# Kernel tuning notes

Hardware: AMD Instinct MI355X
Metric: run time of the kernel (lower is better)

Reference implementation:

```python
import jax, jax.numpy as jnp
import numpy as np

L = 3; D = 128; H = 8; RBF = 16; SBF = 112
N = 60000; E = 300000; A = 8000; G = 256
EPS = 1e-8


def setup_inputs() -> dict:
    key = jax.random.key(0)
    ks = jax.random.split(key, 32)
    p = lambda i, shape: jax.random.normal(ks[i], shape, jnp.float32) * 0.05
    inp = {}
    inp['x'] = jax.random.normal(ks[0], (N, D), jnp.float32)
    inp['node_rbf'] = jax.random.uniform(ks[1], (N, RBF), jnp.float32)
    inp['edge_sbf'] = jax.random.uniform(ks[2], (E, SBF), jnp.float32)
    inp['edge_index'] = jax.random.randint(ks[3], (2, E), 0, N)
    inp['pair_atom_idx'] = jax.random.randint(ks[4], (E,), 0, A)
    inp['edge_index_0'] = jax.random.randint(ks[5], (N,), 0, A)
    inp['atom_batch'] = jnp.sort(jax.random.randint(ks[6], (A,), 0, G))
    inp['batch'] = jnp.sort(jax.random.randint(ks[7], (N,), 0, G))
    inp['edgenn_w1'] = p(8, (L, D, D)); inp['edgenn_b1'] = jnp.zeros((L, D))
    inp['edgenn_w2'] = p(9, (L, D, D)); inp['edgenn_b2'] = jnp.zeros((L, D))
    inp['conv_wq'] = p(10, (L, D, D)); inp['conv_wk'] = p(11, (L, D, D))
    inp['conv_wv'] = p(12, (L, D, D)); inp['conv_we'] = p(13, (L, D, D))
    inp['conv_wsbf'] = p(14, (L, SBF, D)); inp['conv_bsbf'] = jnp.zeros((L, D))
    inp['conv_wrbf'] = p(15, (L, RBF, D))
    inp['dense_w'] = p(16, (L, D, D)); inp['dense_b'] = jnp.zeros((L, D))
    inp['bf_w'] = p(17, (L, 2, D, D)); inp['bf_b'] = jnp.zeros((L, 2, D))
    inp['af_w'] = p(18, (L, 4, D, D)); inp['af_b'] = jnp.zeros((L, 4, D))
    inp['read_wrbf'] = p(19, (L + 1, RBF, D))
    inp['read_w1'] = p(20, (L + 1, D, D)); inp['read_b1'] = jnp.zeros((L + 1, D))
    inp['read_w2'] = p(21, (L + 1, D, D)); inp['read_b2'] = jnp.zeros((L + 1, D))
    inp['read_w3'] = p(22, (L + 1, D, 1)); inp['read_b3'] = jnp.zeros((L + 1, 1))
    return inp


def _forward(x, node_rbf, edge_sbf, edge_index, pair_atom_idx, edge_index_0,
             atom_batch, batch, edgenn_w1, edgenn_b1, edgenn_w2, edgenn_b2,
             conv_wq, conv_wk, conv_wv, conv_we, conv_wsbf, conv_bsbf, conv_wrbf,
             dense_w, dense_b, bf_w, bf_b, af_w, af_b,
             read_wrbf, read_w1, read_b1, read_w2, read_b2, read_w3, read_b3):
    segsum = jax.ops.segment_sum
    silu = jax.nn.silu
    src, dst = edge_index[0], edge_index[1]
    C = D // H

    def readout(i, h):
        # AtomWise: rbf-gated node features, scatter to atoms, small MLP -> [A,1]
        g = h * (node_rbf @ read_wrbf[i])
        atoms = segsum(g, edge_index_0, num_segments=A)
        a = silu(atoms @ read_w1[i] + read_b1[i])
        a = silu(a @ read_w2[i] + read_b2[i])
        return a @ read_w3[i] + read_b3[i]

    def res_block(h, w, b):
        # DimeNet-style ResidualLayer: x + act(lin2(act(lin1(x))))
        return h + silu(silu(h @ w[0] + b[0]) @ w[1] + b[1])

    def graph_norm(h):
        # batch-aware LayerNorm (graph mode, affine=False)
        cnt = segsum(jnp.ones((N,), h.dtype), batch, num_segments=G) * D
        mean = segsum(h.sum(-1), batch, num_segments=G) / cnt
        hc = h - mean[batch][:, None]
        var = segsum((hc * hc).sum(-1), batch, num_segments=G) / cnt
        return hc * jax.lax.rsqrt(var + EPS)[batch][:, None]

    out = x
    results = readout(0, out)
    for i in range(L):
        res0 = out
        atoms_rep = segsum(out, edge_index_0, num_segments=A)  # scatter_add to atoms
        ea = atoms_rep[pair_atom_idx]                           # gather per conv-edge
        ea = silu(ea @ edgenn_w1[i] + edgenn_b1[i]) @ edgenn_w2[i] + edgenn_b2[i]
        # SBFTransformerConv: TransformerConv with sbf-modulated messages + rbf gate
        q = (out @ conv_wq[i]).reshape(N, H, C)
        k = (out @ conv_wk[i]).reshape(N, H, C)
        v = (out @ conv_wv[i]).reshape(N, H, C)
        ek = (ea @ conv_we[i]).reshape(E, H, C)
        kj = k[src] + ek
        logit = (q[dst] * kj).sum(-1) / jnp.sqrt(jnp.asarray(C, out.dtype))  # [E,H]
        m = jax.ops.segment_max(logit, dst, num_segments=N)
        ex = jnp.exp(logit - m[dst])
        alpha = ex / (segsum(ex, dst, num_segments=N)[dst] + 1e-16)
        sw = (edge_sbf @ conv_wsbf[i] + conv_bsbf[i]).reshape(E, H, C)
        msg = (v[src] + ek) * alpha[:, :, None] * sw
        h = segsum(msg, dst, num_segments=N).reshape(N, D)
        out = h * (node_rbf @ conv_wrbf[i])
        out = graph_norm(out)
        out = res_block(out, bf_w[i], bf_b[i])
        out = silu(out @ dense_w[i] + dense_b[i])
        out = out + res0
        out = res_block(out, af_w[i, :2], af_b[i, :2])
        out = res_block(out, af_w[i, 2:], af_b[i, 2:])
        results = results + readout(i + 1, out)
    graphs = segsum(results, atom_batch, num_segments=G)  # [G,1]
    return graphs.reshape(-1) / L


def reference(x, node_rbf, edge_sbf, edge_index, pair_atom_idx, edge_index_0,
              atom_batch, batch, edgenn_w1, edgenn_b1, edgenn_w2, edgenn_b2,
              conv_wq, conv_wk, conv_wv, conv_we, conv_wsbf, conv_bsbf, conv_wrbf,
              dense_w, dense_b, bf_w, bf_b, af_w, af_b,
              read_wrbf, read_w1, read_b1, read_w2, read_b2, read_w3, read_b3):
    return _forward(x, node_rbf, edge_sbf, edge_index, pair_atom_idx, edge_index_0,
                    atom_batch, batch, edgenn_w1, edgenn_b1, edgenn_w2, edgenn_b2,
                    conv_wq, conv_wk, conv_wv, conv_we, conv_wsbf, conv_bsbf, conv_wrbf,
                    dense_w, dense_b, bf_w, bf_b, af_w, af_b,
                    read_wrbf, read_w1, read_b1, read_w2, read_b2, read_w3, read_b3)
```

## Files before the change

kernel.cpp:

```cpp
#include <hip/hip_runtime.h>
#include <math.h>

#define D    128
#define NH   8
#define CPH  16
#define RBFD 16
#define SBFD 112
#define LAYERS 3

typedef __attribute__((ext_vector_type(8))) short bf16x8;
typedef __attribute__((ext_vector_type(4))) float f32x4;

__device__ __forceinline__ float siluf(float x){ return x / (1.0f + __expf(-x)); }

__device__ __forceinline__ short f2bf(float f){
  union { float f; unsigned u; } v; v.f = f;
  unsigned r = v.u + 0x7FFFu + ((v.u >> 16) & 1u);
  return (short)(r >> 16);
}

template<int DIN, int ACT, bool GATHER, bool HASB, bool HASRES>
__global__ __launch_bounds__(256, 2) void k_gemm(
    const float* __restrict__ X, const int* __restrict__ gidx,
    const float* __restrict__ W, const float* __restrict__ bias,
    const float* res, float* __restrict__ Y, int M)
{
  __shared__ short Wt[128 * 128];
  if (DIN < 128){
    for (int i = threadIdx.x; i < 128 * 128; i += 256) Wt[i] = 0;
    __syncthreads();
  }
  for (int i = threadIdx.x; i < DIN * 128; i += 256){
    int k = i >> 7, c = i & 127;
    Wt[c * 128 + k] = f2bf(W[i]);
  }
  __syncthreads();

  const int lane = threadIdx.x & 63;
  const int wave = threadIdx.x >> 6;
  const int col0 = lane & 15;
  const int kg   = lane >> 4;

  bf16x8 Bf[8][4];
  #pragma unroll
  for (int ct = 0; ct < 8; ct++)
    #pragma unroll
    for (int s = 0; s < 4; s++)
      Bf[ct][s] = *(const bf16x8*)&Wt[(ct * 16 + col0) * 128 + s * 32 + kg * 8];

  float bs[8];
  if (HASB){
    #pragma unroll
    for (int ct = 0; ct < 8; ct++) bs[ct] = bias[ct * 16 + col0];
  }

  const long tiles = ((long)M + 63) >> 6;
  for (long t = blockIdx.x; t < tiles; t += gridDim.x){
    const long rbase = t * 64 + wave * 16;
    const long arow  = rbase + col0;
    long srow = 0;
    if (arow < M) srow = GATHER ? (long)gidx[arow] : arow;
    const float* Xp = X + srow * DIN;

    bf16x8 Af[4];
    #pragma unroll
    for (int s = 0; s < 4; s++){
      const int kb = s * 32 + kg * 8;
      bf16x8 a;
      if (DIN == 128 || kb + 8 <= DIN){
        float4 lo = *(const float4*)(Xp + kb);
        float4 hi = *(const float4*)(Xp + kb + 4);
        a[0]=f2bf(lo.x); a[1]=f2bf(lo.y); a[2]=f2bf(lo.z); a[3]=f2bf(lo.w);
        a[4]=f2bf(hi.x); a[5]=f2bf(hi.y); a[6]=f2bf(hi.z); a[7]=f2bf(hi.w);
      } else {
        #pragma unroll
        for (int j = 0; j < 8; j++) a[j] = 0;
      }
      Af[s] = a;
    }

    f32x4 acc[8];
    #pragma unroll
    for (int ct = 0; ct < 8; ct++){ acc[ct][0]=0.f; acc[ct][1]=0.f; acc[ct][2]=0.f; acc[ct][3]=0.f; }
    #pragma unroll
    for (int ct = 0; ct < 8; ct++)
      #pragma unroll
      for (int s = 0; s < 4; s++)
        acc[ct] = __builtin_amdgcn_mfma_f32_16x16x32_bf16(Af[s], Bf[ct][s], acc[ct], 0, 0, 0);

    #pragma unroll
    for (int ct = 0; ct < 8; ct++){
      const int c = ct * 16 + col0;
      #pragma unroll
      for (int r = 0; r < 4; r++){
        const long orow = rbase + kg * 4 + r;
        if (orow < M){
          float v = acc[ct][r];
          if (HASB) v += bs[ct];
          if (ACT)  v = siluf(v);
          if (HASRES) v += res[orow * D + c];
          Y[orow * D + c] = v;
        }
      }
    }
  }
}

__global__ __launch_bounds__(256, 2) void k_gemm2(
    const float* __restrict__ X, const int* __restrict__ gidx,
    const float* __restrict__ W1, const float* __restrict__ b1,
    const float* __restrict__ W2, const float* __restrict__ b2,
    float* __restrict__ Y, int M)
{
  __shared__ short W1t[128 * 128];
  __shared__ short W2t[128 * 128];
  __shared__ short Ts[64 * 128];
  for (int i = threadIdx.x; i < 128 * 128; i += 256){
    int k = i >> 7, c = i & 127;
    W1t[c * 128 + k] = f2bf(W1[i]);
    W2t[c * 128 + k] = f2bf(W2[i]);
  }
  __syncthreads();

  const int lane = threadIdx.x & 63;
  const int wave = threadIdx.x >> 6;
  const int col0 = lane & 15;
  const int kg   = lane >> 4;

  bf16x8 B1f[8][4];
  #pragma unroll
  for (int ct = 0; ct < 8; ct++)
    #pragma unroll
    for (int s = 0; s < 4; s++)
      B1f[ct][s] = *(const bf16x8*)&W1t[(ct * 16 + col0) * 128 + s * 32 + kg * 8];

  float bs1[8], bs2[8];
  #pragma unroll
  for (int ct = 0; ct < 8; ct++){ bs1[ct] = b1[ct * 16 + col0]; bs2[ct] = b2[ct * 16 + col0]; }

  const long tiles = ((long)M + 63) >> 6;
  for (long t = blockIdx.x; t < tiles; t += gridDim.x){
    const long rbase = t * 64 + wave * 16;
    const long arow  = rbase + col0;
    long srow = 0;
    if (arow < M) srow = (long)gidx[arow];
    const float* Xp = X + srow * D;

    bf16x8 Af[4];
    #pragma unroll
    for (int s = 0; s < 4; s++){
      const int kb = s * 32 + kg * 8;
      float4 lo = *(const float4*)(Xp + kb);
      float4 hi = *(const float4*)(Xp + kb + 4);
      bf16x8 a;
      a[0]=f2bf(lo.x); a[1]=f2bf(lo.y); a[2]=f2bf(lo.z); a[3]=f2bf(lo.w);
      a[4]=f2bf(hi.x); a[5]=f2bf(hi.y); a[6]=f2bf(hi.z); a[7]=f2bf(hi.w);
      Af[s] = a;
    }

    f32x4 acc[8];
    #pragma unroll
    for (int ct = 0; ct < 8; ct++){ acc[ct][0]=0.f; acc[ct][1]=0.f; acc[ct][2]=0.f; acc[ct][3]=0.f; }
    #pragma unroll
    for (int ct = 0; ct < 8; ct++)
      #pragma unroll
      for (int s = 0; s < 4; s++)
        acc[ct] = __builtin_amdgcn_mfma_f32_16x16x32_bf16(Af[s], B1f[ct][s], acc[ct], 0, 0, 0);

    #pragma unroll
    for (int ct = 0; ct < 8; ct++){
      const int c = ct * 16 + col0;
      #pragma unroll
      for (int r = 0; r < 4; r++){
        const int row = wave * 16 + kg * 4 + r;
        const int gg = (c >> 3) ^ (row & 7);
        Ts[row * 128 + gg * 8 + (c & 7)] = f2bf(siluf(acc[ct][r] + bs1[ct]));
      }
    }
    __syncthreads();

    const int row2 = wave * 16 + col0;
    bf16x8 A2f[4];
    #pragma unroll
    for (int s = 0; s < 4; s++){
      const int chunk = (s * 4 + kg) ^ (row2 & 7);
      A2f[s] = *(const bf16x8*)&Ts[row2 * 128 + chunk * 8];
    }
    __syncthreads();

    #pragma unroll
    for (int ct = 0; ct < 8; ct++){ acc[ct][0]=0.f; acc[ct][1]=0.f; acc[ct][2]=0.f; acc[ct][3]=0.f; }
    #pragma unroll
    for (int ct = 0; ct < 8; ct++){
      bf16x8 B2v[4];
      #pragma unroll
      for (int s = 0; s < 4; s++)
        B2v[s] = *(const bf16x8*)&W2t[(ct * 16 + col0) * 128 + s * 32 + kg * 8];
      #pragma unroll
      for (int s = 0; s < 4; s++)
        acc[ct] = __builtin_amdgcn_mfma_f32_16x16x32_bf16(A2f[s], B2v[s], acc[ct], 0, 0, 0);
    }

    #pragma unroll
    for (int ct = 0; ct < 8; ct++){
      const int c = ct * 16 + col0;
      #pragma unroll
      for (int r = 0; r < 4; r++){
        const long orow = rbase + kg * 4 + r;
        if (orow < M) Y[orow * D + c] = acc[ct][r] + bs2[ct];
      }
    }
  }
}

__global__ void k_hist(const int* __restrict__ idx, int* __restrict__ cnt, int M)
{
  for (long i = (long)blockIdx.x * 256 + threadIdx.x; i < M; i += (long)gridDim.x * 256)
    atomicAdd(&cnt[idx[i]], 1);
}

__global__ void k_scan(const int* __restrict__ cnt, int* __restrict__ rowptr, int M)
{
  __shared__ int buf[1024];
  const int tid = threadIdx.x;
  const int PT = 16;
  int carry = 0;
  for (int base = 0; base < M; base += 1024 * PT){
    int loc[PT]; int s = 0;
    #pragma unroll
    for (int j = 0; j < PT; j++){
      int i = base + tid * PT + j;
      loc[j] = (i < M) ? cnt[i] : 0;
      s += loc[j];
    }
    buf[tid] = s; __syncthreads();
    for (int off = 1; off < 1024; off <<= 1){
      int t = (tid >= off) ? buf[tid - off] : 0;
      __syncthreads();
      buf[tid] += t;
      __syncthreads();
    }
    int run = buf[tid] - s + carry;
    carry += buf[1023];
    __syncthreads();
    #pragma unroll
    for (int j = 0; j < PT; j++){
      int i = base + tid * PT + j;
      if (i < M) rowptr[i] = run;
      run += loc[j];
    }
  }
  if (tid == 0) rowptr[M] = carry;
}

__global__ void k_fill(const int* __restrict__ idx, const int* __restrict__ rowptr,
                       int* __restrict__ cursor, int* __restrict__ ids, int M)
{
  for (long i = (long)blockIdx.x * 256 + threadIdx.x; i < M; i += (long)gridDim.x * 256){
    int sgm = idx[i];
    int pos = atomicAdd(&cursor[sgm], 1);
    ids[rowptr[sgm] + pos] = (int)i;
  }
}

__global__ __launch_bounds__(256) void k_gather_sum(
    const float* __restrict__ X, const int* __restrict__ rowptr,
    const int* __restrict__ ids, float* __restrict__ Yat, int A_)
{
  const int lane = threadIdx.x & 63;
  const int wv   = threadIdx.x >> 6;
  for (long a = (long)blockIdx.x * 4 + wv; a < A_; a += (long)gridDim.x * 4){
    int beg = rowptr[a], end = rowptr[a + 1];
    float a0 = 0.f, a1 = 0.f;
    for (int i = beg; i < end; i++){
      const float* xp = X + (long)ids[i] * D;
      a0 += xp[lane]; a1 += xp[lane + 64];
    }
    Yat[a * D + lane] = a0; Yat[a * D + lane + 64] = a1;
  }
}

__global__ __launch_bounds__(256) void k_gather_gate_sum(
    const float* __restrict__ X, const float* __restrict__ rbf,
    const float* __restrict__ Wr, const int* __restrict__ rowptr,
    const int* __restrict__ ids, float* __restrict__ Yat, int A_)
{
  __shared__ float Wrs[RBFD * D];
  for (int i = threadIdx.x; i < RBFD * D; i += 256) Wrs[i] = Wr[i];
  __syncthreads();
  const int lane = threadIdx.x & 63;
  const int wv   = threadIdx.x >> 6;
  for (long a = (long)blockIdx.x * 4 + wv; a < A_; a += (long)gridDim.x * 4){
    int beg = rowptr[a], end = rowptr[a + 1];
    float a0 = 0.f, a1 = 0.f;
    for (int i = beg; i < end; i++){
      long n = ids[i];
      const float* xp = X + n * D;
      const float* rb = rbf + n * RBFD;
      float g0 = 0.f, g1 = 0.f;
      #pragma unroll
      for (int r = 0; r < RBFD; r++){
        float rv = rb[r];
        g0 += rv * Wrs[r * D + lane];
        g1 += rv * Wrs[r * D + lane + 64];
      }
      a0 += xp[lane] * g0; a1 += xp[lane + 64] * g1;
    }
    Yat[a * D + lane] = a0; Yat[a * D + lane + 64] = a1;
  }
}

__global__ __launch_bounds__(256) void k_attn(
    float* __restrict__ q, const float* __restrict__ k, const float* __restrict__ v,
    const float* __restrict__ ek, const float* __restrict__ sw,
    const int* __restrict__ rowptr, const int* __restrict__ eids,
    const int* __restrict__ srcA, const float* __restrict__ rbf,
    const float* __restrict__ Wr, const int* __restrict__ batch,
    double* __restrict__ sums, double* __restrict__ sumsq, int Nn)
{
  __shared__ float Wrs[RBFD * D];
  for (int i = threadIdx.x; i < RBFD * D; i += 256) Wrs[i] = Wr[i];
  __syncthreads();
  const int lane = threadIdx.x & 63;
  const int wv   = threadIdx.x >> 6;
  for (long d = (long)blockIdx.x * 4 + wv; d < Nn; d += (long)gridDim.x * 4){
    const int beg = rowptr[d], end = rowptr[d + 1];
    const float q0 = q[d * D + lane], q1 = q[d * D + lane + 64];
    float m0 = -1e30f, m1 = -1e30f, l0 = 0.f, l1 = 0.f, a0 = 0.f, a1 = 0.f;
    for (int i = beg; i < end; i++){
      const long e = eids[i];
      const long s = srcA[e];
      const float* kp = k  + s * D;
      const float* vp = v  + s * D;
      const float* ep = ek + e * D;
      const float* sp = sw + e * D;
      float e0 = ep[lane], e1 = ep[lane + 64];
      float t0 = q0 * (kp[lane] + e0), t1 = q1 * (kp[lane + 64] + e1);
      #pragma unroll
      for (int off = 1; off < 16; off <<= 1){
        t0 += __shfl_xor(t0, off, 64);
        t1 += __shfl_xor(t1, off, 64);
      }
      t0 *= 0.25f; t1 *= 0.25f;
      float u0 = (vp[lane] + e0) * sp[lane];
      float u1 = (vp[lane + 64] + e1) * sp[lane + 64];
      float nm0 = fmaxf(m0, t0), nm1 = fmaxf(m1, t1);
      float sc0 = __expf(m0 - nm0), sc1 = __expf(m1 - nm1);
      float w0 = __expf(t0 - nm0), w1 = __expf(t1 - nm1);
      l0 = l0 * sc0 + w0;  a0 = a0 * sc0 + w0 * u0;  m0 = nm0;
      l1 = l1 * sc1 + w1;  a1 = a1 * sc1 + w1 * u1;  m1 = nm1;
    }
    a0 /= (l0 + 1e-16f); a1 /= (l1 + 1e-16f);
    const float* rb = rbf + d * RBFD;
    float g0 = 0.f, g1 = 0.f;
    #pragma unroll
    for (int r = 0; r < RBFD; r++){
      float rv = rb[r];
      g0 += rv * Wrs[r * D + lane];
      g1 += rv * Wrs[r * D + lane + 64];
    }
    a0 *= g0; a1 *= g1;
    q[d * D + lane] = a0; q[d * D + lane + 64] = a1;
    float ss = a0 + a1, qq = a0 * a0 + a1 * a1;
    #pragma unroll
    for (int off = 1; off < 64; off <<= 1){
      ss += __shfl_xor(ss, off, 64);
      qq += __shfl_xor(qq, off, 64);
    }
    if (lane == 0){
      int g = batch[d];
      atomicAdd(&sums[g], (double)ss);
      atomicAdd(&sumsq[g], (double)qq);
    }
  }
}

__global__ void k_count(const int* __restrict__ batch, int* __restrict__ cnt, int M)
{
  for (long i = (long)blockIdx.x * 256 + threadIdx.x; i < M; i += (long)gridDim.x * 256)
    atomicAdd(&cnt[batch[i]], 1);
}

__global__ void k_norm_final(const double* __restrict__ sums, const double* __restrict__ sumsq,
                             const int* __restrict__ cnt, float* __restrict__ meanG,
                             float* __restrict__ rstdG)
{
  int g = threadIdx.x;
  double c = (double)cnt[g] * (double)D;
  double mean = sums[g] / c;
  double var = sumsq[g] / c - mean * mean;
  meanG[g] = (float)mean;
  rstdG[g] = (float)(1.0 / sqrt(var + 1e-8));
}

__global__ void k_norm_apply(float* __restrict__ Hio, const int* __restrict__ batch,
                             const float* __restrict__ meanG, const float* __restrict__ rstdG, int M)
{
  long total = (long)M * D;
  for (long i = (long)blockIdx.x * 256 + threadIdx.x; i < total; i += (long)gridDim.x * 256){
    long row = i >> 7;
    int g = batch[row];
    Hio[i] = (Hio[i] - meanG[g]) * rstdG[g];
  }
}

__global__ void k_dot3(const float* __restrict__ A2, const float* __restrict__ w3,
                       const float* __restrict__ b3, float* __restrict__ results, int M)
{
  int lane = threadIdx.x & 63;
  long wave = ((long)blockIdx.x * blockDim.x + threadIdx.x) >> 6;
  long nw = ((long)gridDim.x * blockDim.x) >> 6;
  for (long row = wave; row < M; row += nw){
    float a = A2[row * D + lane] * w3[lane] + A2[row * D + lane + 64] * w3[lane + 64];
    for (int off = 32; off > 0; off >>= 1) a += __shfl_down(a, off, 64);
    if (lane == 0) results[row] += a + b3[0];
  }
}

__global__ void k_final(const float* __restrict__ results, const int* __restrict__ ab,
                        float* __restrict__ out, int A_)
{
  int i = blockIdx.x * 256 + threadIdx.x;
  if (i < A_) atomicAdd(&out[ab[i]], results[i] / 3.0f);
}

__global__ void k_w2e(const float* __restrict__ w2, const float* __restrict__ we,
                      float* __restrict__ W2e)
{
  int i = blockIdx.x >> 7;
  int r = blockIdx.x & 127;
  int c = threadIdx.x;
  const float* w2p = w2 + (size_t)i * D * D + (size_t)r * D;
  const float* wep = we + (size_t)i * D * D;
  float acc = 0.f;
  for (int j = 0; j < D; j++) acc += w2p[j] * wep[j * D + c];
  W2e[(size_t)i * D * D + (size_t)r * D + c] = acc;
}

__global__ void k_b2e(const float* __restrict__ b2, const float* __restrict__ we,
                      float* __restrict__ B2e)
{
  int i = blockIdx.x; int c = threadIdx.x;
  float acc = 0.f;
  for (int j = 0; j < D; j++) acc += b2[(size_t)i * D + j] * we[(size_t)i * D * D + j * D + c];
  B2e[(size_t)i * D + c] = acc;
}

extern "C" void kernel_launch(void* const* d_in, const int* in_sizes, int n_in,
                              void* d_out, int out_size, void* d_ws, size_t ws_size,
                              hipStream_t stream)
{
  const float* x          = (const float*)d_in[0];
  const float* node_rbf   = (const float*)d_in[1];
  const float* edge_sbf   = (const float*)d_in[2];
  const int*   edge_index = (const int*)d_in[3];
  const int*   pair_idx   = (const int*)d_in[4];
  const int*   eidx0      = (const int*)d_in[5];
  const int*   atom_batch = (const int*)d_in[6];
  const int*   batch      = (const int*)d_in[7];
  const float* edgenn_w1  = (const float*)d_in[8];
  const float* edgenn_b1  = (const float*)d_in[9];
  const float* edgenn_w2  = (const float*)d_in[10];
  const float* edgenn_b2  = (const float*)d_in[11];
  const float* conv_wq    = (const float*)d_in[12];
  const float* conv_wk    = (const float*)d_in[13];
  const float* conv_wv    = (const float*)d_in[14];
  const float* conv_we    = (const float*)d_in[15];
  const float* conv_wsbf  = (const float*)d_in[16];
  const float* conv_bsbf  = (const float*)d_in[17];
  const float* conv_wrbf  = (const float*)d_in[18];
  const float* dense_w    = (const float*)d_in[19];
  const float* dense_b    = (const float*)d_in[20];
  const float* bf_w       = (const float*)d_in[21];
  const float* bf_b       = (const float*)d_in[22];
  const float* af_w       = (const float*)d_in[23];
  const float* af_b       = (const float*)d_in[24];
  const float* read_wrbf  = (const float*)d_in[25];
  const float* read_w1    = (const float*)d_in[26];
  const float* read_b1    = (const float*)d_in[27];
  const float* read_w2    = (const float*)d_in[28];
  const float* read_b2    = (const float*)d_in[29];
  const float* read_w3    = (const float*)d_in[30];
  const float* read_b3    = (const float*)d_in[31];

  const int N = in_sizes[0] / D;
  const int E = in_sizes[4];
  const int A = in_sizes[6];
  const int G = out_size;

  char* p = (char*)d_ws;
  auto carve = [&](size_t bytes)->char*{ char* r = p; p += (bytes + 255) & ~(size_t)255; return r; };
  float*    EbufA   = (float*)carve((size_t)E * D * 4);
  float*    EbufB   = (float*)carve((size_t)E * D * 4);
  float*    ping0   = (float*)carve((size_t)N * D * 4);
  float*    ping1   = (float*)carve((size_t)N * D * 4);
  float*    bq      = (float*)carve((size_t)N * D * 4);
  float*    bk      = (float*)carve((size_t)N * D * 4);
  float*    bv      = (float*)carve((size_t)N * D * 4);
  float*    bufAtoms= (float*)carve((size_t)A * D * 4);
  float*    a1      = (float*)carve((size_t)A * D * 4);
  float*    a2      = (float*)carve((size_t)A * D * 4);
  float*    results = (float*)carve((size_t)A * 4);
  double*   sumG    = (double*)carve((size_t)G * 8);
  double*   sumsqG  = (double*)carve((size_t)G * 8);
  int*      cntG    = (int*)carve((size_t)G * 4);
  float*    meanG   = (float*)carve((size_t)G * 4);
  float*    rstdG   = (float*)carve((size_t)G * 4);
  float*    W2e     = (float*)carve((size_t)LAYERS * D * D * 4);
  float*    B2e     = (float*)carve((size_t)LAYERS * D * 4);
  int*      rowptrD = (int*)carve((size_t)(N + 1) * 4);
  int*      eidsD   = (int*)carve((size_t)E * 4);
  int*      cntD    = (int*)carve((size_t)N * 4);
  int*      rowptrA = (int*)carve((size_t)(A + 1) * 4);
  int*      idsA    = (int*)carve((size_t)N * 4);
  int*      cntA    = (int*)carve((size_t)A * 4);

  const int* srcA = edge_index;
  const int* dstA = edge_index + E;

  auto ew_grid = [](long total){ long b = (total + 255) / 256; return (int)(b < 4096 ? b : 4096); };
  auto gemm_grid = [](int M){ long t = ((long)M + 63) / 64; return (int)(t < 1024 ? t : 1024); };
  const int gridAttn = (N + 3) / 4;
  const int gridAtom = (A + 3) / 4;

  hipMemsetAsync(cntG, 0, (size_t)G * 4, stream);
  hipMemsetAsync(results, 0, (size_t)A * 4, stream);
  hipMemsetAsync(d_out, 0, (size_t)G * 4, stream);
  k_count<<<ew_grid(N), 256, 0, stream>>>(batch, cntG, N);
  k_w2e<<<LAYERS * D, D, 0, stream>>>(edgenn_w2, conv_we, W2e);
  k_b2e<<<LAYERS, D, 0, stream>>>(edgenn_b2, conv_we, B2e);
  hipMemsetAsync(cntD, 0, (size_t)N * 4, stream);
  k_hist<<<ew_grid(E), 256, 0, stream>>>(dstA, cntD, E);
  k_scan<<<1, 1024, 0, stream>>>(cntD, rowptrD, N);
  hipMemsetAsync(cntD, 0, (size_t)N * 4, stream);
  k_fill<<<ew_grid(E), 256, 0, stream>>>(dstA, rowptrD, cntD, eidsD, E);
  hipMemsetAsync(cntA, 0, (size_t)A * 4, stream);
  k_hist<<<ew_grid(N), 256, 0, stream>>>(eidx0, cntA, N);
  k_scan<<<1, 1024, 0, stream>>>(cntA, rowptrA, A);
  hipMemsetAsync(cntA, 0, (size_t)A * 4, stream);
  k_fill<<<ew_grid(N), 256, 0, stream>>>(eidx0, rowptrA, cntA, idsA, N);

  auto readout = [&](int i, const float* hbuf){
    k_gather_gate_sum<<<gridAtom, 256, 0, stream>>>(hbuf, node_rbf, read_wrbf + (size_t)i * RBFD * D,
                                                    rowptrA, idsA, bufAtoms, A);
    k_gemm<D,1,false,true,false><<<gemm_grid(A),256,0,stream>>>(bufAtoms, nullptr, read_w1 + (size_t)i*D*D, read_b1 + (size_t)i*D, nullptr, a1, A);
    k_gemm<D,1,false,true,false><<<gemm_grid(A),256,0,stream>>>(a1, nullptr, read_w2 + (size_t)i*D*D, read_b2 + (size_t)i*D, nullptr, a2, A);
    k_dot3<<<((A * 64 + 255) / 256), 256, 0, stream>>>(a2, read_w3 + (size_t)i * D, read_b3 + i, results, A);
  };

  readout(0, x);

  const float* cur = x;
  float* pp[2] = {ping0, ping1};
  for (int i = 0; i < LAYERS; i++){
    float* nxt = pp[i & 1];
    const size_t oDD = (size_t)i * D * D;
    k_gather_sum<<<gridAtom, 256, 0, stream>>>(cur, rowptrA, idsA, bufAtoms, A);
    k_gemm2<<<gemm_grid(E),256,0,stream>>>(bufAtoms, pair_idx, edgenn_w1 + oDD, edgenn_b1 + (size_t)i*D,
                                           W2e + oDD, B2e + (size_t)i*D, EbufB, E);
    k_gemm<D,0,false,false,false><<<gemm_grid(N),256,0,stream>>>(cur, nullptr, conv_wq + oDD, nullptr, nullptr, bq, N);
    k_gemm<D,0,false,false,false><<<gemm_grid(N),256,0,stream>>>(cur, nullptr, conv_wk + oDD, nullptr, nullptr, bk, N);
    k_gemm<D,0,false,false,false><<<gemm_grid(N),256,0,stream>>>(cur, nullptr, conv_wv + oDD, nullptr, nullptr, bv, N);
    k_gemm<SBFD,0,false,true,false><<<gemm_grid(E),256,0,stream>>>(edge_sbf, nullptr, conv_wsbf + (size_t)i*SBFD*D, conv_bsbf + (size_t)i*D, nullptr, EbufA, E);
    hipMemsetAsync(sumG, 0, (size_t)G * 8, stream);
    hipMemsetAsync(sumsqG, 0, (size_t)G * 8, stream);
    k_attn<<<gridAttn, 256, 0, stream>>>(bq, bk, bv, EbufB, EbufA, rowptrD, eidsD, srcA,
                                         node_rbf, conv_wrbf + (size_t)i*RBFD*D, batch,
                                         sumG, sumsqG, N);
    k_norm_final<<<1, G, 0, stream>>>(sumG, sumsqG, cntG, meanG, rstdG);
    k_norm_apply<<<ew_grid((long)N * D), 256, 0, stream>>>(bq, batch, meanG, rstdG, N);
    k_gemm<D,1,false,true,false><<<gemm_grid(N),256,0,stream>>>(bq, nullptr, bf_w + (size_t)i*2*D*D, bf_b + (size_t)i*2*D, nullptr, bk, N);
    k_gemm<D,1,false,true,true ><<<gemm_grid(N),256,0,stream>>>(bk, nullptr, bf_w + (size_t)i*2*D*D + D*D, bf_b + (size_t)i*2*D + D, bq, bq, N);
    k_gemm<D,1,false,true,true ><<<gemm_grid(N),256,0,stream>>>(bq, nullptr, dense_w + oDD, dense_b + (size_t)i*D, cur, nxt, N);
    k_gemm<D,1,false,true,false><<<gemm_grid(N),256,0,stream>>>(nxt, nullptr, af_w + (size_t)i*4*D*D,         af_b + (size_t)i*4*D,       nullptr, bk, N);
    k_gemm<D,1,false,true,true ><<<gemm_grid(N),256,0,stream>>>(bk, nullptr, af_w + (size_t)i*4*D*D + D*D,   af_b + (size_t)i*4*D + D,   nxt, nxt, N);
    k_gemm<D,1,false,true,false><<<gemm_grid(N),256,0,stream>>>(nxt, nullptr, af_w + (size_t)i*4*D*D + 2*D*D, af_b + (size_t)i*4*D + 2*D, nullptr, bk, N);
    k_gemm<D,1,false,true,true ><<<gemm_grid(N),256,0,stream>>>(bk, nullptr, af_w + (size_t)i*4*D*D + 3*D*D, af_b + (size_t)i*4*D + 3*D, nxt, nxt, N);
    readout(i + 1, nxt);
    cur = nxt;
  }
  k_final<<<(A + 255) / 256, 256, 0, stream>>>(results, atom_batch, (float*)d_out, A);
}
```

Before: 3.462 ms.

## Fuse res-block GEMM pairs and readout MLP, permute edge outputs to CSR order

Result: faster. 3.255 ms (-6.0%).

```diff
diff --git a/kernel.cpp b/kernel.cpp
--- a/kernel.cpp
+++ b/kernel.cpp
@@ -19,11 +19,11 @@
   return (short)(r >> 16);
 }
 
-template<int DIN, int ACT, bool GATHER, bool HASB, bool HASRES>
+template<int DIN, int ACT, bool GATHER, bool HASB, bool HASRES, bool PERM>
 __global__ __launch_bounds__(256, 2) void k_gemm(
     const float* __restrict__ X, const int* __restrict__ gidx,
     const float* __restrict__ W, const float* __restrict__ bias,
-    const float* res, float* __restrict__ Y, int M)
+    const float* res, float* __restrict__ Y, const int* __restrict__ operm, int M)
 {
   __shared__ short Wt[128 * 128];
   if (DIN < 128){
@@ -89,18 +89,18 @@
         acc[ct] = __builtin_amdgcn_mfma_f32_16x16x32_bf16(Af[s], Bf[ct][s], acc[ct], 0, 0, 0);
 
     #pragma unroll
-    for (int ct = 0; ct < 8; ct++){
-      const int c = ct * 16 + col0;
-      #pragma unroll
-      for (int r = 0; r < 4; r++){
-        const long orow = rbase + kg * 4 + r;
-        if (orow < M){
-          float v = acc[ct][r];
-          if (HASB) v += bs[ct];
-          if (ACT)  v = siluf(v);
-          if (HASRES) v += res[orow * D + c];
-          Y[orow * D + c] = v;
-        }
+    for (int r = 0; r < 4; r++){
+      const long orow = rbase + kg * 4 + r;
+      if (orow >= M) continue;
+      const long wrow = PERM ? (long)operm[orow] : orow;
+      #pragma unroll
+      for (int ct = 0; ct < 8; ct++){
+        const int c = ct * 16 + col0;
+        float v = acc[ct][r];
+        if (HASB) v += bs[ct];
+        if (ACT)  v = siluf(v);
+        if (HASRES) v += res[orow * D + c];
+        Y[wrow * D + c] = v;
       }
     }
   }
@@ -110,7 +110,7 @@
     const float* __restrict__ X, const int* __restrict__ gidx,
     const float* __restrict__ W1, const float* __restrict__ b1,
     const float* __restrict__ W2, const float* __restrict__ b2,
-    float* __restrict__ Y, int M)
+    float* __restrict__ Y, const int* __restrict__ operm, int M)
 {
   __shared__ short W1t[128 * 128];
   __shared__ short W2t[128 * 128];
@@ -202,13 +202,242 @@
     }
 
     #pragma unroll
+    for (int r = 0; r < 4; r++){
+      const long orow = rbase + kg * 4 + r;
+      if (orow >= M) continue;
+      const long wrow = (long)operm[orow];
+      #pragma unroll
+      for (int ct = 0; ct < 8; ct++){
+        const int c = ct * 16 + col0;
+        Y[wrow * D + c] = acc[ct][r] + bs2[ct];
+      }
+    }
+  }
+}
+
+template<bool NORM>
+__global__ __launch_bounds__(256, 2) void k_res2(
+    const float* __restrict__ X,
+    const float* __restrict__ W1, const float* __restrict__ b1,
+    const float* __restrict__ W2, const float* __restrict__ b2,
+    const int* __restrict__ batch, const float* __restrict__ meanG,
+    const float* __restrict__ rstdG, float* __restrict__ Y, int M)
+{
+  __shared__ short W1t[128 * 128];
+  __shared__ short W2t[128 * 128];
+  __shared__ short Ts[64 * 128];
+  for (int i = threadIdx.x; i < 128 * 128; i += 256){
+    int k = i >> 7, c = i & 127;
+    W1t[c * 128 + k] = f2bf(W1[i]);
+    W2t[c * 128 + k] = f2bf(W2[i]);
+  }
+  __syncthreads();
+
+  const int lane = threadIdx.x & 63;
+  const int wave = threadIdx.x >> 6;
+  const int col0 = lane & 15;
+  const int kg   = lane >> 4;
+
+  bf16x8 B1f[8][4];
+  #pragma unroll
+  for (int ct = 0; ct < 8; ct++)
+    #pragma unroll
+    for (int s = 0; s < 4; s++)
+      B1f[ct][s] = *(const bf16x8*)&W1t[(ct * 16 + col0) * 128 + s * 32 + kg * 8];
+
+  float bs1[8], bs2[8];
+  #pragma unroll
+  for (int ct = 0; ct < 8; ct++){ bs1[ct] = b1[ct * 16 + col0]; bs2[ct] = b2[ct * 16 + col0]; }
+
+  const long tiles = ((long)M + 63) >> 6;
+  for (long t = blockIdx.x; t < tiles; t += gridDim.x){
+    const long rbase = t * 64 + wave * 16;
+    const long arow  = rbase + col0;
+    const float* Xp = X + (arow < M ? arow : 0) * D;
+    float xm = 0.f, xr = 1.f;
+    if (NORM && arow < M){ int g = batch[arow]; xm = meanG[g]; xr = rstdG[g]; }
+
+    bf16x8 Af[4];
+    #pragma unroll
+    for (int s = 0; s < 4; s++){
+      const int kb = s * 32 + kg * 8;
+      float4 lo = *(const float4*)(Xp + kb);
+      float4 hi = *(const float4*)(Xp + kb + 4);
+      bf16x8 a;
+      a[0]=f2bf((lo.x-xm)*xr); a[1]=f2bf((lo.y-xm)*xr); a[2]=f2bf((lo.z-xm)*xr); a[3]=f2bf((lo.w-xm)*xr);
+      a[4]=f2bf((hi.x-xm)*xr); a[5]=f2bf((hi.y-xm)*xr); a[6]=f2bf((hi.z-xm)*xr); a[7]=f2bf((hi.w-xm)*xr);
+      Af[s] = a;
+    }
+
+    f32x4 acc[8];
+    #pragma unroll
+    for (int ct = 0; ct < 8; ct++){ acc[ct][0]=0.f; acc[ct][1]=0.f; acc[ct][2]=0.f; acc[ct][3]=0.f; }
+    #pragma unroll
+    for (int ct = 0; ct < 8; ct++)
+      #pragma unroll
+      for (int s = 0; s < 4; s++)
+        acc[ct] = __builtin_amdgcn_mfma_f32_16x16x32_bf16(Af[s], B1f[ct][s], acc[ct], 0, 0, 0);
+
+    #pragma unroll
     for (int ct = 0; ct < 8; ct++){
       const int c = ct * 16 + col0;
       #pragma unroll
       for (int r = 0; r < 4; r++){
-        const long orow = rbase + kg * 4 + r;
-        if (orow < M) Y[orow * D + c] = acc[ct][r] + bs2[ct];
+        const int row = wave * 16 + kg * 4 + r;
+        const int gg = (c >> 3) ^ (row & 7);
+        Ts[row * 128 + gg * 8 + (c & 7)] = f2bf(siluf(acc[ct][r] + bs1[ct]));
       }
+    }
+    __syncthreads();
+
+    const int row2 = wave * 16 + col0;
+    bf16x8 A2f[4];
+    #pragma unroll
+    for (int s = 0; s < 4; s++){
+      const int chunk = (s * 4 + kg) ^ (row2 & 7);
+      A2f[s] = *(const bf16x8*)&Ts[row2 * 128 + chunk * 8];
+    }
+    __syncthreads();
+
+    #pragma unroll
+    for (int ct = 0; ct < 8; ct++){ acc[ct][0]=0.f; acc[ct][1]=0.f; acc[ct][2]=0.f; acc[ct][3]=0.f; }
+    #pragma unroll
+    for (int ct = 0; ct < 8; ct++){
+      bf16x8 B2v[4];
+      #pragma unroll
+      for (int s = 0; s < 4; s++)
+        B2v[s] = *(const bf16x8*)&W2t[(ct * 16 + col0) * 128 + s * 32 + kg * 8];
+      #pragma unroll
+      for (int s = 0; s < 4; s++)
+        acc[ct] = __builtin_amdgcn_mfma_f32_16x16x32_bf16(A2f[s], B2v[s], acc[ct], 0, 0, 0);
+    }
+
+    #pragma unroll
+    for (int r = 0; r < 4; r++){
+      const long orow = rbase + kg * 4 + r;
+      if (orow >= M) continue;
+      float rm = 0.f, rr = 1.f;
+      if (NORM){ int g = batch[orow]; rm = meanG[g]; rr = rstdG[g]; }
+      #pragma unroll
+      for (int ct = 0; ct < 8; ct++){
+        const int c = ct * 16 + col0;
+        float base = X[orow * D + c];
+        if (NORM) base = (base - rm) * rr;
+        Y[orow * D + c] = base + siluf(acc[ct][r] + bs2[ct]);
+      }
+    }
+  }
+}
+
+__global__ __launch_bounds__(256, 2) void k_read2(
+    const float* __restrict__ X,
+    const float* __restrict__ W1, const float* __restrict__ b1,
+    const float* __restrict__ W2, const float* __restrict__ b2,
+    const float* __restrict__ w3, const float* __restrict__ b3,
+    float* __restrict__ results, int M)
+{
+  __shared__ short W1t[128 * 128];
+  __shared__ short W2t[128 * 128];
+  __shared__ short Ts[64 * 128];
+  for (int i = threadIdx.x; i < 128 * 128; i += 256){
+    int k = i >> 7, c = i & 127;
+    W1t[c * 128 + k] = f2bf(W1[i]);
+    W2t[c * 128 + k] = f2bf(W2[i]);
+  }
+  __syncthreads();
+
+  const int lane = threadIdx.x & 63;
+  const int wave = threadIdx.x >> 6;
+  const int col0 = lane & 15;
+  const int kg   = lane >> 4;
+
+  bf16x8 B1f[8][4];
+  #pragma unroll
+  for (int ct = 0; ct < 8; ct++)
+    #pragma unroll
+    for (int s = 0; s < 4; s++)
+      B1f[ct][s] = *(const bf16x8*)&W1t[(ct * 16 + col0) * 128 + s * 32 + kg * 8];
+
+  float bs1[8], bs2[8], w3v[8];
+  #pragma unroll
+  for (int ct = 0; ct < 8; ct++){
+    bs1[ct] = b1[ct * 16 + col0];
+    bs2[ct] = b2[ct * 16 + col0];
+    w3v[ct] = w3[ct * 16 + col0];
+  }
+  const float b3v = b3[0];
+
+  const long tiles = ((long)M + 63) >> 6;
+  for (long t = blockIdx.x; t < tiles; t += gridDim.x){
+    const long rbase = t * 64 + wave * 16;
+    const long arow  = rbase + col0;
+    const float* Xp = X + (arow < M ? arow : 0) * D;
+
+    bf16x8 Af[4];
+    #pragma unroll
+    for (int s = 0; s < 4; s++){
+      const int kb = s * 32 + kg * 8;
+      float4 lo = *(const float4*)(Xp + kb);
+      float4 hi = *(const float4*)(Xp + kb + 4);
+      bf16x8 a;
+      a[0]=f2bf(lo.x); a[1]=f2bf(lo.y); a[2]=f2bf(lo.z); a[3]=f2bf(lo.w);
+      a[4]=f2bf(hi.x); a[5]=f2bf(hi.y); a[6]=f2bf(hi.z); a[7]=f2bf(hi.w);
+      Af[s] = a;
+    }
+
+    f32x4 acc[8];
+    #pragma unroll
+    for (int ct = 0; ct < 8; ct++){ acc[ct][0]=0.f; acc[ct][1]=0.f; acc[ct][2]=0.f; acc[ct][3]=0.f; }
+    #pragma unroll
+    for (int ct = 0; ct < 8; ct++)
+      #pragma unroll
+      for (int s = 0; s < 4; s++)
+        acc[ct] = __builtin_amdgcn_mfma_f32_16x16x32_bf16(Af[s], B1f[ct][s], acc[ct], 0, 0, 0);
+
+    #pragma unroll
+    for (int ct = 0; ct < 8; ct++){
+      const int c = ct * 16 + col0;
+      #pragma unroll
+      for (int r = 0; r < 4; r++){
+        const int row = wave * 16 + kg * 4 + r;
+        const int gg = (c >> 3) ^ (row & 7);
+        Ts[row * 128 + gg * 8 + (c & 7)] = f2bf(siluf(acc[ct][r] + bs1[ct]));
+      }
+    }
+    __syncthreads();
+
+    const int row2 = wave * 16 + col0;
+    bf16x8 A2f[4];
+    #pragma unroll
+    for (int s = 0; s < 4; s++){
+      const int chunk = (s * 4 + kg) ^ (row2 & 7);
+      A2f[s] = *(const bf16x8*)&Ts[row2 * 128 + chunk * 8];
+    }
+    __syncthreads();
+
+    #pragma unroll
+    for (int ct = 0; ct < 8; ct++){ acc[ct][0]=0.f; acc[ct][1]=0.f; acc[ct][2]=0.f; acc[ct][3]=0.f; }
+    #pragma unroll
+    for (int ct = 0; ct < 8; ct++){
+      bf16x8 B2v[4];
+      #pragma unroll
+      for (int s = 0; s < 4; s++)
+        B2v[s] = *(const bf16x8*)&W2t[(ct * 16 + col0) * 128 + s * 32 + kg * 8];
+      #pragma unroll
+      for (int s = 0; s < 4; s++)
+        acc[ct] = __builtin_amdgcn_mfma_f32_16x16x32_bf16(A2f[s], B2v[s], acc[ct], 0, 0, 0);
+    }
+
+    #pragma unroll
+    for (int r = 0; r < 4; r++){
+      float vr = 0.f;
+      #pragma unroll
+      for (int ct = 0; ct < 8; ct++)
+        vr += siluf(acc[ct][r] + bs2[ct]) * w3v[ct];
+      #pragma unroll
+      for (int off = 1; off < 16; off <<= 1) vr += __shfl_xor(vr, off, 64);
+      const long orow = rbase + kg * 4 + r;
+      if (col0 == 0 && orow < M) results[orow] += vr + b3v;
     }
   }
 }
@@ -260,6 +489,16 @@
     int sgm = idx[i];
     int pos = atomicAdd(&cursor[sgm], 1);
     ids[rowptr[sgm] + pos] = (int)i;
+  }
+}
+
+__global__ void k_invsrc(const int* __restrict__ eids, const int* __restrict__ srcA,
+                         int* __restrict__ invD, int* __restrict__ srcCSR, int E_)
+{
+  for (long i = (long)blockIdx.x * 256 + threadIdx.x; i < E_; i += (long)gridDim.x * 256){
+    int e = eids[i];
+    invD[e] = (int)i;
+    srcCSR[i] = srcA[e];
   }
 }
 
@@ -310,12 +549,39 @@
   }
 }
 
+__device__ __forceinline__ void attn_step(long i, const int* __restrict__ srcCSR,
+    const float* __restrict__ k, const float* __restrict__ v,
+    const float* __restrict__ ek, const float* __restrict__ sw, int lane,
+    float q0, float q1, float& m0, float& m1, float& l0, float& l1, float& a0, float& a1)
+{
+  const long s = srcCSR[i];
+  const float* kp = k + s * D;
+  const float* vp = v + s * D;
+  const float* ep = ek + i * D;
+  const float* sp = sw + i * D;
+  float e0 = ep[lane], e1 = ep[lane + 64];
+  float t0 = q0 * (kp[lane] + e0), t1 = q1 * (kp[lane + 64] + e1);
+  #pragma unroll
+  for (int off = 1; off < 16; off <<= 1){
+    t0 += __shfl_xor(t0, off, 64);
+    t1 += __shfl_xor(t1, off, 64);
+  }
+  t0 *= 0.25f; t1 *= 0.25f;
+  float u0 = (vp[lane] + e0) * sp[lane];
+  float u1 = (vp[lane + 64] + e1) * sp[lane + 64];
+  float nm0 = fmaxf(m0, t0), nm1 = fmaxf(m1, t1);
+  float sc0 = __expf(m0 - nm0), sc1 = __expf(m1 - nm1);
+  float w0 = __expf(t0 - nm0), w1 = __expf(t1 - nm1);
+  l0 = l0 * sc0 + w0;  a0 = a0 * sc0 + w0 * u0;  m0 = nm0;
+  l1 = l1 * sc1 + w1;  a1 = a1 * sc1 + w1 * u1;  m1 = nm1;
+}
+
 __global__ __launch_bounds__(256) void k_attn(
     float* __restrict__ q, const float* __restrict__ k, const float* __restrict__ v,
     const float* __restrict__ ek, const float* __restrict__ sw,
-    const int* __restrict__ rowptr, const int* __restrict__ eids,
-    const int* __restrict__ srcA, const float* __restrict__ rbf,
-    const float* __restrict__ Wr, const int* __restrict__ batch,
+    const int* __restrict__ rowptr, const int* __restrict__ srcCSR,
+    const float* __restrict__ rbf, const float* __restrict__ Wr,
+    const int* __restrict__ batch,
     double* __restrict__ sums, double* __restrict__ sumsq, int Nn)
 {
   __shared__ float Wrs[RBFD * D];
@@ -326,30 +592,20 @@
   for (long d = (long)blockIdx.x * 4 + wv; d < Nn; d += (long)gridDim.x * 4){
     const int beg = rowptr[d], end = rowptr[d + 1];
     const float q0 = q[d * D + lane], q1 = q[d * D + lane + 64];
-    float m0 = -1e30f, m1 = -1e30f, l0 = 0.f, l1 = 0.f, a0 = 0.f, a1 = 0.f;
-    for (int i = beg; i < end; i++){
-      const long e = eids[i];
-      const long s = srcA[e];
-      const float* kp = k  + s * D;
-      const float* vp = v  + s * D;
-      const float* ep = ek + e * D;
-      const float* sp = sw + e * D;
-      float e0 = ep[lane], e1 = ep[lane + 64];
-      float t0 = q0 * (kp[lane] + e0), t1 = q1 * (kp[lane + 64] + e1);
-      #pragma unroll
-      for (int off = 1; off < 16; off <<= 1){
-        t0 += __shfl_xor(t0, off, 64);
-        t1 += __shfl_xor(t1, off, 64);
-      }
-      t0 *= 0.25f; t1 *= 0.25f;
-      float u0 = (vp[lane] + e0) * sp[lane];
-      float u1 = (vp[lane + 64] + e1) * sp[lane + 64];
-      float nm0 = fmaxf(m0, t0), nm1 = fmaxf(m1, t1);
-      float sc0 = __expf(m0 - nm0), sc1 = __expf(m1 - nm1);
-      float w0 = __expf(t0 - nm0), w1 = __expf(t1 - nm1);
-      l0 = l0 * sc0 + w0;  a0 = a0 * sc0 + w0 * u0;  m0 = nm0;
-      l1 = l1 * sc1 + w1;  a1 = a1 * sc1 + w1 * u1;  m1 = nm1;
-    }
+    float mA0=-1e30f, mA1=-1e30f, lA0=0.f, lA1=0.f, aA0=0.f, aA1=0.f;
+    float mB0=-1e30f, mB1=-1e30f, lB0=0.f, lB1=0.f, aB0=0.f, aB1=0.f;
+    int i = beg;
+    for (; i + 1 < end; i += 2){
+      attn_step(i,     srcCSR, k, v, ek, sw, lane, q0, q1, mA0, mA1, lA0, lA1, aA0, aA1);
+      attn_step(i + 1, srcCSR, k, v, ek, sw, lane, q0, q1, mB0, mB1, lB0, lB1, aB0, aB1);
+    }
+    if (i < end)
+      attn_step(i, srcCSR, k, v, ek, sw, lane, q0, q1, mA0, mA1, lA0, lA1, aA0, aA1);
+    float nm0 = fmaxf(mA0, mB0), nm1 = fmaxf(mA1, mB1);
+    float sA0 = __expf(mA0 - nm0), sB0 = __expf(mB0 - nm0);
+    float sA1 = __expf(mA1 - nm1), sB1 = __expf(mB1 - nm1);
+    float l0 = lA0 * sA0 + lB0 * sB0, l1 = lA1 * sA1 + lB1 * sB1;
+    float a0 = aA0 * sA0 + aB0 * sB0, a1 = aA1 * sA1 + aB1 * sB1;
     a0 /= (l0 + 1e-16f); a1 /= (l1 + 1e-16f);
     const float* rb = rbf + d * RBFD;
     float g0 = 0.f, g1 = 0.f;
@@ -391,30 +647,6 @@
   double var = sumsq[g] / c - mean * mean;
   meanG[g] = (float)mean;
   rstdG[g] = (float)(1.0 / sqrt(var + 1e-8));
-}
-
-__global__ void k_norm_apply(float* __restrict__ Hio, const int* __restrict__ batch,
-                             const float* __restrict__ meanG, const float* __restrict__ rstdG, int M)
-{
-  long total = (long)M * D;
-  for (long i = (long)blockIdx.x * 256 + threadIdx.x; i < total; i += (long)gridDim.x * 256){
-    long row = i >> 7;
-    int g = batch[row];
-    Hio[i] = (Hio[i] - meanG[g]) * rstdG[g];
-  }
-}
-
-__global__ void k_dot3(const float* __restrict__ A2, const float* __restrict__ w3,
-                       const float* __restrict__ b3, float* __restrict__ results, int M)
-{
-  int lane = threadIdx.x & 63;
-  long wave = ((long)blockIdx.x * blockDim.x + threadIdx.x) >> 6;
-  long nw = ((long)gridDim.x * blockDim.x) >> 6;
-  for (long row = wave; row < M; row += nw){
-    float a = A2[row * D + lane] * w3[lane] + A2[row * D + lane + 64] * w3[lane + 64];
-    for (int off = 32; off > 0; off >>= 1) a += __shfl_down(a, off, 64);
-    if (lane == 0) results[row] += a + b3[0];
-  }
 }
 
 __global__ void k_final(const float* __restrict__ results, const int* __restrict__ ab,
@@ -498,8 +730,6 @@
   float*    bk      = (float*)carve((size_t)N * D * 4);
   float*    bv      = (float*)carve((size_t)N * D * 4);
   float*    bufAtoms= (float*)carve((size_t)A * D * 4);
-  float*    a1      = (float*)carve((size_t)A * D * 4);
-  float*    a2      = (float*)carve((size_t)A * D * 4);
   float*    results = (float*)carve((size_t)A * 4);
   double*   sumG    = (double*)carve((size_t)G * 8);
   double*   sumsqG  = (double*)carve((size_t)G * 8);
@@ -510,6 +740,8 @@
   float*    B2e     = (float*)carve((size_t)LAYERS * D * 4);
   int*      rowptrD = (int*)carve((size_t)(N + 1) * 4);
   int*      eidsD   = (int*)carve((size_t)E * 4);
+  int*      invD    = (int*)carve((size_t)E * 4);
+  int*      srcCSR  = (int*)carve((size_t)E * 4);
   int*      cntD    = (int*)carve((size_t)N * 4);
   int*      rowptrA = (int*)carve((size_t)(A + 1) * 4);
   int*      idsA    = (int*)carve((size_t)N * 4);
@@ -534,6 +766,7 @@
   k_scan<<<1, 1024, 0, stream>>>(cntD, rowptrD, N);
   hipMemsetAsync(cntD, 0, (size_t)N * 4, stream);
   k_fill<<<ew_grid(E), 256, 0, stream>>>(dstA, rowptrD, cntD, eidsD, E);
+  k_invsrc<<<ew_grid(E), 256, 0, stream>>>(eidsD, srcA, invD, srcCSR, E);
   hipMemsetAsync(cntA, 0, (size_t)A * 4, stream);
   k_hist<<<ew_grid(N), 256, 0, stream>>>(eidx0, cntA, N);
   k_scan<<<1, 1024, 0, stream>>>(cntA, rowptrA, A);
@@ -543,9 +776,10 @@
   auto readout = [&](int i, const float* hbuf){
     k_gather_gate_sum<<<gridAtom, 256, 0, stream>>>(hbuf, node_rbf, read_wrbf + (size_t)i * RBFD * D,
                                                     rowptrA, idsA, bufAtoms, A);
-    k_gemm<D,1,false,true,false><<<gemm_grid(A),256,0,stream>>>(bufAtoms, nullptr, read_w1 + (size_t)i*D*D, read_b1 + (size_t)i*D, nullptr, a1, A);
-    k_gemm<D,1,false,true,false><<<gemm_grid(A),256,0,stream>>>(a1, nullptr, read_w2 + (size_t)i*D*D, read_b2 + (size_t)i*D, nullptr, a2, A);
-    k_dot3<<<((A * 64 + 255) / 256), 256, 0, stream>>>(a2, read_w3 + (size_t)i * D, read_b3 + i, results, A);
+    k_read2<<<gemm_grid(A), 256, 0, stream>>>(bufAtoms,
+        read_w1 + (size_t)i*D*D, read_b1 + (size_t)i*D,
+        read_w2 + (size_t)i*D*D, read_b2 + (size_t)i*D,
+        read_w3 + (size_t)i*D, read_b3 + i, results, A);
   };
 
   readout(0, x);
@@ -557,25 +791,26 @@
     const size_t oDD = (size_t)i * D * D;
     k_gather_sum<<<gridAtom, 256, 0, stream>>>(cur, rowptrA, idsA, bufAtoms, A);
     k_gemm2<<<gemm_grid(E),256,0,stream>>>(bufAtoms, pair_idx, edgenn_w1 + oDD, edgenn_b1 + (size_t)i*D,
-                                           W2e + oDD, B2e + (size_t)i*D, EbufB, E);
-    k_gemm<D,0,false,false,false><<<gemm_grid(N),256,0,stream>>>(cur, nullptr, conv_wq + oDD, nullptr, nullptr, bq, N);
-    k_gemm<D,0,false,false,false><<<gemm_grid(N),256,0,stream>>>(cur, nullptr, conv_wk + oDD, nullptr, nullptr, bk, N);
-    k_gemm<D,0,false,false,false><<<gemm_grid(N),256,0,stream>>>(cur, nullptr, conv_wv + oDD, nullptr, nullptr, bv, N);
-    k_gemm<SBFD,0,false,true,false><<<gemm_grid(E),256,0,stream>>>(edge_sbf, nullptr, conv_wsbf + (size_t)i*SBFD*D, conv_bsbf + (size_t)i*D, nullptr, EbufA, E);
-    hipMemsetAsync(sumG, 0, (size_t)G * 8, stream);
-    hipMemsetAsync(sumsqG, 0, (size_t)G * 8, stream);
-    k_attn<<<gridAttn, 256, 0, stream>>>(bq, bk, bv, EbufB, EbufA, rowptrD, eidsD, srcA,
+                                           W2e + oDD, B2e + (size_t)i*D, EbufB, invD, E);
+    k_gemm<D,0,false,false,false,false><<<gemm_grid(N),256,0,stream>>>(cur, nullptr, conv_wq + oDD, nullptr, nullptr, bq, nullptr, N);
+    k_gemm<D,0,false,false,false,false><<<gemm_grid(N),256,0,stream>>>(cur, nullptr, conv_wk + oDD, nullptr, nullptr, bk, nullptr, N);
+    k_gemm<D,0,false,false,false,false><<<gemm_grid(N),256,0,stream>>>(cur, nullptr, conv_wv + oDD, nullptr, nullptr, bv, nullptr, N);
+    k_gemm<SBFD,0,false,true,false,true><<<gemm_grid(E),256,0,stream>>>(edge_sbf, nullptr, conv_wsbf + (size_t)i*SBFD*D, conv_bsbf + (size_t)i*D, nullptr, EbufA, invD, E);
+    hipMemsetAsync(sumG, 0, (size_t)G * 16, stream);
+    k_attn<<<gridAttn, 256, 0, stream>>>(bq, bk, bv, EbufB, EbufA, rowptrD, srcCSR,
                                          node_rbf, conv_wrbf + (size_t)i*RBFD*D, batch,
                                          sumG, sumsqG, N);
     k_norm_final<<<1, G, 0, stream>>>(sumG, sumsqG, cntG, meanG, rstdG);
-    k_norm_apply<<<ew_grid((long)N * D), 256, 0, stream>>>(bq, batch, meanG, rstdG, N);
-    k_gemm<D,1,false,true,false><<<gemm_grid(N),256,0,stream>>>(bq, nullptr, bf_w + (size_t)i*2*D*D, bf_b + (size_t)i*2*D, nullptr, bk, N);
-    k_gemm<D,1,false,true,true ><<<gemm_grid(N),256,0,stream>>>(bk, nullptr, bf_w + (size_t)i*2*D*D + D*D, bf_b + (size_t)i*2*D + D, bq, bq, N);
-    k_gemm<D,1,false,true,true ><<<gemm_grid(N),256,0,stream>>>(bq, nullptr, dense_w + oDD, dense_b + (size_t)i*D, cur, nxt, N);
-    k_gemm<D,1,false,true,false><<<gemm_grid(N),256,0,stream>>>(nxt, nullptr, af_w + (size_t)i*4*D*D,         af_b + (size_t)i*4*D,       nullptr, bk, N);
-    k_gemm<D,1,false,true,true ><<<gemm_grid(N),256,0,stream>>>(bk, nullptr, af_w + (size_t)i*4*D*D + D*D,   af_b + (size_t)i*4*D + D,   nxt, nxt, N);
-    k_gemm<D,1,false,true,false><<<gemm_grid(N),256,0,stream>>>(nxt, nullptr, af_w + (size_t)i*4*D*D + 2*D*D, af_b + (size_t)i*4*D + 2*D, nullptr, bk, N);
-    k_gemm<D,1,false,true,true ><<<gemm_grid(N),256,0,stream>>>(bk, nullptr, af_w + (size_t)i*4*D*D + 3*D*D, af_b + (size_t)i*4*D + 3*D, nxt, nxt, N);
+    k_res2<true><<<gemm_grid(N),256,0,stream>>>(bq, bf_w + (size_t)i*2*D*D, bf_b + (size_t)i*2*D,
+                                                bf_w + (size_t)i*2*D*D + D*D, bf_b + (size_t)i*2*D + D,
+                                                batch, meanG, rstdG, bq, N);
+    k_gemm<D,1,false,true,true,false><<<gemm_grid(N),256,0,stream>>>(bq, nullptr, dense_w + oDD, dense_b + (size_t)i*D, cur, nxt, nullptr, N);
+    k_res2<false><<<gemm_grid(N),256,0,stream>>>(nxt, af_w + (size_t)i*4*D*D,         af_b + (size_t)i*4*D,
+                                                 af_w + (size_t)i*4*D*D + D*D,       af_b + (size_t)i*4*D + D,
+                                                 nullptr, nullptr, nullptr, nxt, N);
+    k_res2<false><<<gemm_grid(N),256,0,stream>>>(nxt, af_w + (size_t)i*4*D*D + 2*D*D, af_b + (size_t)i*4*D + 2*D,
+                                                 af_w + (size_t)i*4*D*D + 3*D*D,     af_b + (size_t)i*4*D + 3*D,
+                                                 nullptr, nullptr, nullptr, nxt, N);
     readout(i + 1, nxt);
     cur = nxt;
   }
```
